# Kernel tuning notes

Measured on AMD Instinct MI355X. Metric: run time of the kernel, lower is better.

The kernel has to match this reference:

```python
import jax, jax.numpy as jnp
import numpy as np
from jax import lax

T, D, I, E = 4096, 1024, 1024, 32
TOP_K = 4
ROUTED_SCALING = 1.0
EPS = 1e-6


def setup_inputs() -> dict:
    key = jax.random.key(0)
    k1, k2, k3, k4, k5 = jax.random.split(key, 5)
    return {
        "hidden_states": jax.random.normal(k1, (T, D), dtype=jnp.float32),
        "gate_w": jax.random.normal(k2, (E, D), dtype=jnp.float32) * 0.02,
        "gate_up_proj": jax.random.normal(k3, (E, 2 * I, D), dtype=jnp.float32) * 0.02,
        "down_proj": jax.random.normal(k4, (E, D, I), dtype=jnp.float32) * 0.02,
        "expert_bias": jax.random.normal(k5, (E,), dtype=jnp.float32) * 0.01,
    }


def _route(hidden_states, gate_w, expert_bias):
    # router_logits: [T, E]
    logits = hidden_states @ gate_w.T
    routing_weights = jax.nn.sigmoid(logits)
    # expert bias affects selection only, not the weights
    scores = routing_weights + expert_bias[None, :]
    _, selected = lax.top_k(scores, TOP_K)                      # [T, K] int32
    w = jnp.take_along_axis(routing_weights, selected, axis=1)  # [T, K]
    w = w / (w.sum(axis=-1, keepdims=True) + EPS)               # norm_topk_prob
    w = w * ROUTED_SCALING
    return selected, w


def reference(hidden_states, gate_w, gate_up_proj, down_proj, expert_bias):
    t, d = hidden_states.shape
    selected, w = _route(hidden_states, gate_w, expert_bias)
    # dense token->expert combine weights [T, E] (top_k indices are unique per row)
    comb = jnp.zeros((t, E), dtype=hidden_states.dtype)
    comb = comb.at[jnp.arange(t)[:, None], selected].add(w)

    def body(acc, xs):
        w_gu, w_d, cw = xs                       # [2I,D], [D,I], [T]
        gu = hidden_states @ w_gu.T              # [T, 2I]
        g, u = jnp.split(gu, 2, axis=-1)
        h = jax.nn.silu(g) * u                   # [T, I]
        out = h @ w_d.T                          # [T, D]
        return acc + out * cw[:, None], None

    init = jnp.zeros_like(hidden_states)
    final, _ = lax.scan(body, init, (gate_up_proj, down_proj, comb.T))
    return final
```

## Files before the change

kernel.cpp:

```cpp
#include <hip/hip_runtime.h>
#include <hip/hip_bf16.h>
#include <cstdint>
#include <cstddef>

#define T_TOK 4096
#define DIM   1024
#define IDIM  1024
#define NEXP  32
#define TOPK  4
#define MAXT  160
#define RPAD  (MAXT*128)
#define G1_BLOCKS (MAXT*16)
#define CONV_BLOCKS 8192

typedef short sh8   __attribute__((ext_vector_type(8)));
typedef float f32x4 __attribute__((ext_vector_type(4)));

__device__ __forceinline__ short bf(float f) {
    union { float f; uint32_t u; } v; v.f = f;
    uint32_t r = (v.u + 0x7FFFu + ((v.u >> 16) & 1u)) >> 16;
    return (short)r;
}
__device__ __forceinline__ sh8 pack8(float4 a, float4 b) {
    sh8 r;
    r[0]=bf(a.x); r[1]=bf(a.y); r[2]=bf(a.z); r[3]=bf(a.w);
    r[4]=bf(b.x); r[5]=bf(b.y); r[6]=bf(b.z); r[7]=bf(b.w);
    return r;
}
__device__ __forceinline__ uint32_t cvtpk(float lo, float hi) {
    uint32_t r;
    asm("v_cvt_pk_bf16_f32 %0, %1, %2" : "=v"(r) : "v"(lo), "v"(hi));
    return r;
}
__device__ __forceinline__ sh8 cvt8(f32x4 a, f32x4 b) {
    union { uint32_t u[4]; sh8 s; } v;
    v.u[0] = cvtpk(a[0], a[1]); v.u[1] = cvtpk(a[2], a[3]);
    v.u[2] = cvtpk(b[0], b[1]); v.u[3] = cvtpk(b[2], b[3]);
    return v.s;
}
__device__ __forceinline__ void glds16(const void* g, const void* l) {
    __builtin_amdgcn_global_load_lds((const __attribute__((address_space(1))) void*)g,
                                     (__attribute__((address_space(3))) void*)l, 16, 0, 0);
}

__device__ __forceinline__ int tile_expert(const int* __restrict__ cnt, int mt, int& tile_start) {
    int s = 0, e = -1, ts = 0;
    #pragma unroll
    for (int i = 0; i < NEXP; ++i) {
        int t = (cnt[i] + 127) >> 7;
        if (mt >= s && mt < s + t) { e = i; ts = s; }
        s += t;
    }
    tile_start = ts;
    return e;
}

__device__ __forceinline__ int balanced_bid(const int* __restrict__ cnt, int ntsz) {
    int tb = 0;
    #pragma unroll
    for (int i = 0; i < NEXP; ++i) tb += (cnt[i] + 127) >> 7;
    int total = tb * ntsz;
    int q = total >> 3, r = total & 7;
    int xcd = (int)blockIdx.x & 7, pos = (int)blockIdx.x >> 3;
    int cap = q + (xcd < r ? 1 : 0);
    if (pos >= cap) return -1;
    return (xcd < r ? xcd * (q + 1) : r * (q + 1) + (xcd - r) * q) + pos;
}

__device__ __forceinline__ bool decode_wmajor(const int* __restrict__ cnt, int bid, int ntsz,
                                              int& e, int& mt, int& nt) {
    int base = 0, tacc = 0, fe = -1, floc = 0, fts = 0, fntl = 1;
    #pragma unroll
    for (int i = 0; i < NEXP; ++i) {
        int ntl = (cnt[i] + 127) >> 7;
        int sz  = ntsz * ntl;
        if (bid >= base && bid < base + sz) { fe = i; floc = bid - base; fts = tacc; fntl = ntl; }
        base += sz; tacc += ntl;
    }
    if (fe < 0) return false;
    e  = fe;
    nt = floc / fntl;
    mt = fts + (floc % fntl);
    return true;
}

__global__ __launch_bounds__(256) void router_kernel(
    const float* __restrict__ X, const float* __restrict__ GW,
    const float* __restrict__ bias, int* __restrict__ topk_idx,
    float* __restrict__ topk_w, int* __restrict__ cnt,
    int* __restrict__ tlist_c, int* __restrict__ posmap)
{
    int wid  = threadIdx.x >> 6;
    int lane = threadIdx.x & 63;
    int t = blockIdx.x * 4 + wid;

    float4 h[4];
    const float4* xr = reinterpret_cast<const float4*>(X + (size_t)t * DIM);
    #pragma unroll
    for (int c = 0; c < 4; ++c) h[c] = xr[lane + 64 * c];

    float myscore = 0.f;
    for (int e = 0; e < NEXP; ++e) {
        const float4* gr = reinterpret_cast<const float4*>(GW + (size_t)e * DIM);
        float p = 0.f;
        #pragma unroll
        for (int c = 0; c < 4; ++c) {
            float4 g = gr[lane + 64 * c];
            p += h[c].x * g.x + h[c].y * g.y + h[c].z * g.z + h[c].w * g.w;
        }
        #pragma unroll
        for (int o = 32; o; o >>= 1) p += __shfl_xor(p, o);
        if (lane == e) myscore = p;
    }
    float rw = 1.f / (1.f + expf(-myscore));
    float sel = (lane < NEXP) ? rw + bias[lane] : -1e30f;

    float wsum = 0.f;
    int   oi = 0; float ow = 0.f;
    #pragma unroll
    for (int k = 0; k < TOPK; ++k) {
        float v = sel;
        int   idx = (lane < NEXP) ? lane : 9999;
        #pragma unroll
        for (int o = 32; o; o >>= 1) {
            float v2 = __shfl_xor(v, o);
            int   i2 = __shfl_xor(idx, o);
            if (v2 > v || (v2 == v && i2 < idx)) { v = v2; idx = i2; }
        }
        float wk = __shfl(rw, idx);
        wsum += wk;
        if (lane == k)   { oi = idx; ow = wk; }
        if (lane == idx) sel = -1e30f;
    }
    if (lane < TOPK) {
        int gid = t * TOPK + lane;
        topk_idx[gid] = oi;
        topk_w  [gid] = ow / (wsum + 1e-6f);
        int pos = atomicAdd(&cnt[oi], 1);
        tlist_c[oi * T_TOK + pos] = t;
        posmap[gid] = pos;
    }
}

__global__ __launch_bounds__(256) void gather_kernel(
    const float* __restrict__ X, const int* __restrict__ cnt,
    const int* __restrict__ tlist_c, short* __restrict__ Xg)
{
    int wid = threadIdx.x >> 6, lane = threadIdx.x & 63;
    int r = blockIdx.x * 4 + wid;
    int ts;
    int e = tile_expert(cnt, r >> 7, ts);
    if (e < 0) return;
    int li = r - (ts << 7);
    bool real = li < cnt[e];
    int t = real ? tlist_c[e * T_TOK + li] : 0;
    const float4* src = reinterpret_cast<const float4*>(X + (size_t)t * DIM);
    sh8* dst = reinterpret_cast<sh8*>(Xg + (size_t)r * DIM);
    float4 z = make_float4(0.f, 0.f, 0.f, 0.f);
    #pragma unroll
    for (int it = 0; it < 2; ++it) {
        int si = it * 64 + lane;
        float4 a = real ? src[2 * si]     : z;
        float4 b = real ? src[2 * si + 1] : z;
        dst[si] = pack8(a, b);
    }
}

__global__ __launch_bounds__(256, 3) void gemm1_kernel(
    const short* __restrict__ Xg, const float* __restrict__ GUP,
    const float* __restrict__ DP, short* __restrict__ Wdb,
    const int* __restrict__ cnt, short* __restrict__ H)
{
    if (blockIdx.x >= G1_BLOCKS) {
        size_t i = ((size_t)(blockIdx.x - G1_BLOCKS) * 256 + threadIdx.x) * 16;
        f32x4 a = *reinterpret_cast<const f32x4*>(DP + i);
        f32x4 b = *reinterpret_cast<const f32x4*>(DP + i + 4);
        f32x4 c = *reinterpret_cast<const f32x4*>(DP + i + 8);
        f32x4 d = *reinterpret_cast<const f32x4*>(DP + i + 12);
        *reinterpret_cast<sh8*>(Wdb + i)     = cvt8(a, b);
        *reinterpret_cast<sh8*>(Wdb + i + 8) = cvt8(c, d);
        return;
    }
    int bid = balanced_bid(cnt, 16);
    if (bid < 0) return;
    int e, mt, nt;
    if (!decode_wmajor(cnt, bid, 16, e, mt, nt)) return;
    int m0 = mt * 128, n0 = nt * 64;

    __shared__ short As[128 * 64];
    __shared__ float Bg[64 * 64];
    __shared__ float Bu[64 * 64];

    int tid = threadIdx.x, lane = tid & 63, wv = tid >> 6;
    int wm = (wv >> 1) * 64, wn = (wv & 1) * 32;

    f32x4 accg[4][2] = {};
    f32x4 accu[4][2] = {};

    int swcolA = ((lane & 7) ^ (lane >> 3)) * 8;
    const float* gbase = GUP + ((size_t)e * 2 * IDIM + n0) * DIM;
    const float* ubase = gbase + (size_t)IDIM * DIM;

    auto stage = [&](int k0) {
        #pragma unroll
        for (int j = 0; j < 4; ++j) {
            int ch = wv * 4 + j;
            glds16(Xg + (size_t)(m0 + ch * 8 + (lane >> 3)) * DIM + k0 + swcolA, &As[ch * 512]);
        }
        #pragma unroll
        for (int j = 0; j < 4; ++j) {
            int ch = wv * 4 + j;
            int r  = ch * 4 + (lane >> 4);
            int sc = ((lane & 15) ^ (r & 15)) << 2;
            glds16(gbase + (size_t)r * DIM + k0 + sc, &Bg[ch * 256]);
            glds16(ubase + (size_t)r * DIM + k0 + sc, &Bu[ch * 256]);
        }
    };

    int swrA = (lane & 7) << 3;
    int rx   = lane & 15;
    for (int it = 0; it < DIM / 64; ++it) {
        stage(it * 64);
        __syncthreads();
        #pragma unroll
        for (int kk = 0; kk < 64; kk += 32) {
            int kiA = (kk + (lane >> 4) * 8) ^ swrA;
            sh8 af[4], gf[2], uf[2];
            #pragma unroll
            for (int fm = 0; fm < 4; ++fm)
                af[fm] = *reinterpret_cast<const sh8*>(&As[(wm + fm * 16 + (lane & 15)) * 64 + kiA]);
            int c0 = (kk >> 2) + (lane >> 4) * 2;
            #pragma unroll
            for (int fn = 0; fn < 2; ++fn) {
                int R = wn + fn * 16 + (lane & 15);
                const float* bg = &Bg[R * 64];
                f32x4 lo = *reinterpret_cast<const f32x4*>(&bg[(c0       ^ rx) << 2]);
                f32x4 hi = *reinterpret_cast<const f32x4*>(&bg[((c0 + 1) ^ rx) << 2]);
                gf[fn] = cvt8(lo, hi);
                const float* bu = &Bu[R * 64];
                lo = *reinterpret_cast<const f32x4*>(&bu[(c0       ^ rx) << 2]);
                hi = *reinterpret_cast<const f32x4*>(&bu[((c0 + 1) ^ rx) << 2]);
                uf[fn] = cvt8(lo, hi);
            }
            #pragma unroll
            for (int fm = 0; fm < 4; ++fm)
                #pragma unroll
                for (int fn = 0; fn < 2; ++fn) {
                    accg[fm][fn] = __builtin_amdgcn_mfma_f32_16x16x32_bf16(af[fm], gf[fn], accg[fm][fn], 0, 0, 0);
                    accu[fm][fn] = __builtin_amdgcn_mfma_f32_16x16x32_bf16(af[fm], uf[fn], accu[fm][fn], 0, 0, 0);
                }
        }
        __syncthreads();
    }

    #pragma unroll
    for (int fm = 0; fm < 4; ++fm)
        #pragma unroll
        for (int r = 0; r < 4; ++r) {
            int row = m0 + wm + fm * 16 + (lane >> 4) * 4 + r;
            #pragma unroll
            for (int fn = 0; fn < 2; ++fn) {
                int col = n0 + wn + fn * 16 + (lane & 15);
                float g = accg[fm][fn][r];
                float u = accu[fm][fn][r];
                H[(size_t)row * IDIM + col] = bf(g / (1.f + expf(-g)) * u);
            }
        }
}

__global__ __launch_bounds__(256, 3) void gemm2_kernel(
    const short* __restrict__ H, const short* __restrict__ Wdb,
    const int* __restrict__ cnt, float* __restrict__ Yf)
{
    int bid = balanced_bid(cnt, 8);
    if (bid < 0) return;
    int e, mt, nt;
    if (!decode_wmajor(cnt, bid, 8, e, mt, nt)) return;
    int m0 = mt * 128, n0 = nt * 128;

    __shared__ short As[128 * 64];
    __shared__ short Bs[128 * 64];

    int tid = threadIdx.x, lane = tid & 63, wv = tid >> 6;
    int wm = (wv >> 1) * 64, wn = (wv & 1) * 64;
    int l15 = lane & 15;

    f32x4 acc[4][4] = {};

    int swcolA = ((lane & 7) ^ (lane >> 3)) * 8;
    const short* bbase = Wdb + ((size_t)e * DIM + n0) * IDIM;

    auto stage = [&](int k0) {
        #pragma unroll
        for (int j = 0; j < 4; ++j) {
            int ch = wv * 4 + j;
            glds16(H + (size_t)(m0 + ch * 8 + (lane >> 3)) * IDIM + k0 + swcolA, &As[ch * 512]);
        }
        #pragma unroll
        for (int j = 0; j < 4; ++j) {
            int ch = wv * 4 + j;
            glds16(bbase + (size_t)(ch * 8 + (lane >> 3)) * IDIM + k0 + swcolA, &Bs[ch * 512]);
        }
    };

    int swr = (lane & 7) << 3;
    for (int it = 0; it < IDIM / 64; ++it) {
        stage(it * 64);
        __syncthreads();
        #pragma unroll
        for (int kk = 0; kk < 64; kk += 32) {
            int ki = (kk + (lane >> 4) * 8) ^ swr;
            sh8 af[4], bq[4];
            #pragma unroll
            for (int fm = 0; fm < 4; ++fm)
                af[fm] = *reinterpret_cast<const sh8*>(&As[(wm + fm * 16 + l15) * 64 + ki]);
            #pragma unroll
            for (int fn = 0; fn < 4; ++fn)
                bq[fn] = *reinterpret_cast<const sh8*>(&Bs[(wn + fn * 16 + l15) * 64 + ki]);
            #pragma unroll
            for (int fm = 0; fm < 4; ++fm)
                #pragma unroll
                for (int fn = 0; fn < 4; ++fn)
                    acc[fm][fn] = __builtin_amdgcn_mfma_f32_16x16x32_bf16(af[fm], bq[fn], acc[fm][fn], 0, 0, 0);
        }
        __syncthreads();
    }

    #pragma unroll
    for (int fm = 0; fm < 4; ++fm)
        #pragma unroll
        for (int r = 0; r < 4; ++r) {
            int row = m0 + wm + fm * 16 + (lane >> 4) * 4 + r;
            #pragma unroll
            for (int fn = 0; fn < 4; ++fn) {
                int col = n0 + wn + fn * 16 + l15;
                Yf[(size_t)row * DIM + col] = acc[fm][fn][r];
            }
        }
}

__global__ __launch_bounds__(256) void combine_kernel(
    const float* __restrict__ Yf, const int* __restrict__ cnt,
    const int* __restrict__ topk_idx, const float* __restrict__ topk_w,
    const int* __restrict__ posmap, float* __restrict__ out)
{
    int t = blockIdx.x;
    int d = threadIdx.x * 4;
    int es[TOPK], rows[TOPK];
    #pragma unroll
    for (int k = 0; k < TOPK; ++k) es[k] = topk_idx[t * TOPK + k];
    int p = 0;
    #pragma unroll
    for (int i = 0; i < NEXP; ++i) {
        #pragma unroll
        for (int k = 0; k < TOPK; ++k)
            if (es[k] == i) rows[k] = p + posmap[t * TOPK + k];
        p += ((cnt[i] + 127) >> 7) << 7;
    }
    float4 acc = make_float4(0.f, 0.f, 0.f, 0.f);
    #pragma unroll
    for (int k = 0; k < TOPK; ++k) {
        float w = topk_w[t * TOPK + k];
        float4 y = *reinterpret_cast<const float4*>(Yf + (size_t)rows[k] * DIM + d);
        acc.x += w * y.x; acc.y += w * y.y; acc.z += w * y.z; acc.w += w * y.w;
    }
    *reinterpret_cast<float4*>(out + (size_t)t * DIM + d) = acc;
}

extern "C" void kernel_launch(void* const* d_in, const int* in_sizes, int n_in,
                              void* d_out, int out_size, void* d_ws, size_t ws_size,
                              hipStream_t stream)
{
    const float* X    = (const float*)d_in[0];
    const float* GW   = (const float*)d_in[1];
    const float* GUP  = (const float*)d_in[2];
    const float* DP   = (const float*)d_in[3];
    const float* BIAS = (const float*)d_in[4];
    float* out = (float*)d_out;

    char* ws = (char*)d_ws;
    int*   cnt      = (int*)ws;
    int*   topk_idx = (int*)(ws + (4u   << 10));
    float* topk_w   = (float*)(ws + (68u  << 10));
    int*   posmap   = (int*)(ws + (132u << 10));
    int*   tlist_c  = (int*)(ws + (196u << 10));

    constexpr size_t OFF_H   = 2ull << 20;
    constexpr size_t SZ_BF   = (size_t)RPAD * IDIM * 2;
    constexpr size_t OFF_XG  = OFF_H + SZ_BF;
    constexpr size_t OFF_YF  = OFF_XG + SZ_BF;
    constexpr size_t OFF_WDB = 192ull << 20;

    short* H   = (short*)(ws + OFF_H);
    short* Xg  = (short*)(ws + OFF_XG);
    float* Yf  = (float*)(ws + OFF_YF);
    short* Wdb = (short*)(ws + OFF_WDB);

    (void)hipMemsetAsync(cnt, 0, 128, stream);

    router_kernel<<<T_TOK / 4, 256, 0, stream>>>(X, GW, BIAS, topk_idx, topk_w,
                                                 cnt, tlist_c, posmap);
    gather_kernel<<<RPAD / 4, 256, 0, stream>>>(X, cnt, tlist_c, Xg);

    gemm1_kernel<<<G1_BLOCKS + CONV_BLOCKS, 256, 0, stream>>>(Xg, GUP, DP, Wdb, cnt, H);
    gemm2_kernel<<<MAXT * 8, 256, 0, stream>>>(H, Wdb, cnt, Yf);

    combine_kernel<<<T_TOK, 256, 0, stream>>>(Yf, cnt, topk_idx, topk_w, posmap, out);
}
```

Baseline: 334.0 us.

## Enlarge gemm1 M-tile to 256 rows per block to halve weight streaming

Gemm1 now covers 256 token rows per block instead of 128, grouping pairs of 128-row tiles within each expert. Each block streams the fp32 gate/up weight tiles once for twice as many rows, so weight traffic and per-tile conversion cost are roughly halved. The last odd tile's loads are clamped to the expert's end and stores are masked. Accumulators double, so launch bounds drop to 2 blocks per SM, which raises register pressure and lowers occupancy. Fewer blocks may also leave some CUs idle.

```diff
diff --git a/kernel.cpp b/kernel.cpp
--- a/kernel.cpp
+++ b/kernel.cpp
@@ -10,7 +10,8 @@
 #define TOPK  4
 #define MAXT  160
 #define RPAD  (MAXT*128)
-#define G1_BLOCKS (MAXT*16)
+#define MAXT2 96
+#define G1_BLOCKS (MAXT2*16)
 #define CONV_BLOCKS 8192
 
 typedef short sh8   __attribute__((ext_vector_type(8)));
@@ -55,11 +56,7 @@
     return e;
 }
 
-__device__ __forceinline__ int balanced_bid(const int* __restrict__ cnt, int ntsz) {
-    int tb = 0;
-    #pragma unroll
-    for (int i = 0; i < NEXP; ++i) tb += (cnt[i] + 127) >> 7;
-    int total = tb * ntsz;
+__device__ __forceinline__ int balanced_map(int total) {
     int q = total >> 3, r = total & 7;
     int xcd = (int)blockIdx.x & 7, pos = (int)blockIdx.x >> 3;
     int cap = q + (xcd < r ? 1 : 0);
@@ -166,7 +163,7 @@
     }
 }
 
-__global__ __launch_bounds__(256, 3) void gemm1_kernel(
+__global__ __launch_bounds__(256, 2) void gemm1_kernel(
     const short* __restrict__ Xg, const float* __restrict__ GUP,
     const float* __restrict__ DP, short* __restrict__ Wdb,
     const int* __restrict__ cnt, short* __restrict__ H)
@@ -181,21 +178,38 @@
         *reinterpret_cast<sh8*>(Wdb + i + 8) = cvt8(c, d);
         return;
     }
-    int bid = balanced_bid(cnt, 16);
+    int tb = 0;
+    #pragma unroll
+    for (int i = 0; i < NEXP; ++i) { int n1 = (cnt[i] + 127) >> 7; tb += (n1 + 1) >> 1; }
+    int bid = balanced_map(tb * 16);
     if (bid < 0) return;
-    int e, mt, nt;
-    if (!decode_wmajor(cnt, bid, 16, e, mt, nt)) return;
-    int m0 = mt * 128, n0 = nt * 64;
-
-    __shared__ short As[128 * 64];
+    int base = 0, ts128 = 0;
+    int e = -1, loc = 0, fts = 0, fn128 = 1, fn256 = 1;
+    #pragma unroll
+    for (int i = 0; i < NEXP; ++i) {
+        int n1 = (cnt[i] + 127) >> 7;
+        int n2 = (n1 + 1) >> 1;
+        int sz = 16 * n2;
+        if (bid >= base && bid < base + sz) { e = i; loc = bid - base; fts = ts128; fn128 = n1; fn256 = n2; }
+        base += sz; ts128 += n1;
+    }
+    if (e < 0) return;
+    int nt = loc / fn256;
+    int lt = loc % fn256;
+    int m0   = (fts + lt * 2) * 128;
+    int eEnd = (fts + fn128) * 128;
+    int n0 = nt * 64;
+
+    __shared__ short As[256 * 64];
     __shared__ float Bg[64 * 64];
     __shared__ float Bu[64 * 64];
 
     int tid = threadIdx.x, lane = tid & 63, wv = tid >> 6;
-    int wm = (wv >> 1) * 64, wn = (wv & 1) * 32;
-
-    f32x4 accg[4][2] = {};
-    f32x4 accu[4][2] = {};
+    int wm = (wv >> 1) * 128, wn = (wv & 1) * 32;
+    int l15 = lane & 15;
+
+    f32x4 accg[8][2] = {};
+    f32x4 accu[8][2] = {};
 
     int swcolA = ((lane & 7) ^ (lane >> 3)) * 8;
     const float* gbase = GUP + ((size_t)e * 2 * IDIM + n0) * DIM;
@@ -203,9 +217,11 @@
 
     auto stage = [&](int k0) {
         #pragma unroll
-        for (int j = 0; j < 4; ++j) {
-            int ch = wv * 4 + j;
-            glds16(Xg + (size_t)(m0 + ch * 8 + (lane >> 3)) * DIM + k0 + swcolA, &As[ch * 512]);
+        for (int j = 0; j < 8; ++j) {
+            int ch = wv * 8 + j;
+            int cr = m0 + ch * 8;
+            if (cr + 8 > eEnd) cr = eEnd - 8;
+            glds16(Xg + (size_t)(cr + (lane >> 3)) * DIM + k0 + swcolA, &As[ch * 512]);
         }
         #pragma unroll
         for (int j = 0; j < 4; ++j) {
@@ -218,21 +234,21 @@
     };
 
     int swrA = (lane & 7) << 3;
-    int rx   = lane & 15;
+    int rx   = l15;
     for (int it = 0; it < DIM / 64; ++it) {
         stage(it * 64);
         __syncthreads();
         #pragma unroll
         for (int kk = 0; kk < 64; kk += 32) {
             int kiA = (kk + (lane >> 4) * 8) ^ swrA;
-            sh8 af[4], gf[2], uf[2];
-            #pragma unroll
-            for (int fm = 0; fm < 4; ++fm)
-                af[fm] = *reinterpret_cast<const sh8*>(&As[(wm + fm * 16 + (lane & 15)) * 64 + kiA]);
+            sh8 af[8], gf[2], uf[2];
+            #pragma unroll
+            for (int fm = 0; fm < 8; ++fm)
+                af[fm] = *reinterpret_cast<const sh8*>(&As[(wm + fm * 16 + l15) * 64 + kiA]);
             int c0 = (kk >> 2) + (lane >> 4) * 2;
             #pragma unroll
             for (int fn = 0; fn < 2; ++fn) {
-                int R = wn + fn * 16 + (lane & 15);
+                int R = wn + fn * 16 + l15;
                 const float* bg = &Bg[R * 64];
                 f32x4 lo = *reinterpret_cast<const f32x4*>(&bg[(c0       ^ rx) << 2]);
                 f32x4 hi = *reinterpret_cast<const f32x4*>(&bg[((c0 + 1) ^ rx) << 2]);
@@ -243,7 +259,7 @@
                 uf[fn] = cvt8(lo, hi);
             }
             #pragma unroll
-            for (int fm = 0; fm < 4; ++fm)
+            for (int fm = 0; fm < 8; ++fm)
                 #pragma unroll
                 for (int fn = 0; fn < 2; ++fn) {
                     accg[fm][fn] = __builtin_amdgcn_mfma_f32_16x16x32_bf16(af[fm], gf[fn], accg[fm][fn], 0, 0, 0);
@@ -254,13 +270,14 @@
     }
 
     #pragma unroll
-    for (int fm = 0; fm < 4; ++fm)
+    for (int fm = 0; fm < 8; ++fm)
         #pragma unroll
         for (int r = 0; r < 4; ++r) {
             int row = m0 + wm + fm * 16 + (lane >> 4) * 4 + r;
+            if (row >= eEnd) continue;
             #pragma unroll
             for (int fn = 0; fn < 2; ++fn) {
-                int col = n0 + wn + fn * 16 + (lane & 15);
+                int col = n0 + wn + fn * 16 + l15;
                 float g = accg[fm][fn][r];
                 float u = accu[fm][fn][r];
                 H[(size_t)row * IDIM + col] = bf(g / (1.f + expf(-g)) * u);
@@ -272,7 +289,10 @@
     const short* __restrict__ H, const short* __restrict__ Wdb,
     const int* __restrict__ cnt, float* __restrict__ Yf)
 {
-    int bid = balanced_bid(cnt, 8);
+    int tb = 0;
+    #pragma unroll
+    for (int i = 0; i < NEXP; ++i) tb += (cnt[i] + 127) >> 7;
+    int bid = balanced_map(tb * 8);
     if (bid < 0) return;
     int e, mt, nt;
     if (!decode_wmajor(cnt, bid, 8, e, mt, nt)) return;
```

After: 338.7 us. Within noise of the previous version (+1.4%).
